# Kernel tuning notes

Measured on AMD Instinct MI355X. Metric: run time of the kernel, lower is better.

Reference implementation:

```python
import jax, jax.numpy as jnp
import numpy as np
from jax import lax

VOCAB, EMB, FILT, ATT, KW = 50000, 300, 400, 200, 3
B, N = 4096, 30

def setup_inputs() -> dict:
    key = jax.random.key(0)
    ks = jax.random.split(key, 7)
    encoded_title = jax.random.randint(ks[0], (B, N), 0, VOCAB)
    emb = jax.random.normal(ks[1], (VOCAB, EMB), dtype=jnp.float32) * 0.1
    conv_w = jax.random.normal(ks[2], (FILT, EMB, KW), dtype=jnp.float32) * (1.0 / np.sqrt(EMB * KW))
    conv_b = jnp.zeros((FILT,), dtype=jnp.float32)
    v = jax.random.normal(ks[3], (FILT, ATT), dtype=jnp.float32) * (1.0 / np.sqrt(FILT))
    vb = jnp.zeros((ATT,), dtype=jnp.float32)
    q = jax.random.normal(ks[4], (ATT, 1), dtype=jnp.float32) * (1.0 / np.sqrt(ATT))
    return {"encoded_title": encoded_title, "emb": emb, "conv_w": conv_w,
            "conv_b": conv_b, "v": v, "vb": vb, "q": q}

def reference(encoded_title, emb, conv_w, conv_b, v, vb, q):
    mask = (encoded_title != 0).astype(jnp.float32)          # [B, N]
    W = emb[encoded_title]                                    # [B, N, E]
    x = jnp.transpose(W, (0, 2, 1))                           # [B, E, N]
    C = lax.conv_general_dilated(x, conv_w, window_strides=(1,),
                                 padding=[(1, 1)],
                                 dimension_numbers=("NCH", "OIH", "NCH"))
    C = jnp.transpose(C, (0, 2, 1)) + conv_b                  # [B, N, F]
    C = jax.nn.relu(C)
    a = jnp.tanh(C @ v + vb)                                  # [B, N, A]
    a = (a @ q)[..., 0]                                       # [B, N]
    alpha = jax.nn.softmax(a, axis=0)                         # softmax over batch dim (faithful to dim=0)
    alpha = alpha * mask
    e = jnp.einsum("bn,bnf->bf", alpha, C)                    # batched weighted-sum pooling
    return e
```

## Files before the change

kernel.cpp:

```cpp
#include <hip/hip_runtime.h>
#include <hip/hip_bf16.h>

#define VOCAB 50000
#define EMB   300
#define FILT  400
#define ATT   200
#define BB    4096
#define NN    30

#define ATTP  208
#define KC    416

typedef short bf16x8 __attribute__((ext_vector_type(8)));
typedef float f32x4  __attribute__((ext_vector_type(4)));
typedef unsigned short u16x4 __attribute__((ext_vector_type(4)));

static __device__ __forceinline__ unsigned short f2bf(float f) {
    __hip_bfloat16 h = __float2bfloat16(f);
    union { __hip_bfloat16 h; unsigned short u; } c; c.h = h; return c.u;
}
static __device__ __forceinline__ float bf2f(unsigned short u) {
    union { unsigned int u; float f; } c; c.u = ((unsigned int)u) << 16; return c.f;
}
static __device__ __forceinline__ float fast_tanh(float x) {
    float e = __expf(2.f * x);
    return 1.f - 2.f * __builtin_amdgcn_rcpf(e + 1.f);
}

static __device__ __forceinline__ void dma16(const unsigned short* g, unsigned short* l) {
    __builtin_amdgcn_global_load_lds(
        (const __attribute__((address_space(1))) unsigned int*)(const void*)g,
        (__attribute__((address_space(3))) unsigned int*)(void*)l,
        16, 0, 0);
}

#define CFENCE() asm volatile("" ::: "memory")
static __device__ __forceinline__ void bar_lgkm0() {
    asm volatile("s_waitcnt lgkmcnt(0)" ::: "memory");
    __builtin_amdgcn_s_barrier();
    CFENCE();
}
static __device__ __forceinline__ void bar_plain() {
    CFENCE();
    __builtin_amdgcn_s_barrier();
    CFENCE();
}

__global__ __launch_bounds__(256) void kP(const float* __restrict__ conv_w,
                                          const float* __restrict__ v,
                                          const float* __restrict__ vb,
                                          const float* __restrict__ q,
                                          unsigned short* __restrict__ Bc2,
                                          unsigned short* __restrict__ Bv2,
                                          float* __restrict__ vbp,
                                          float* __restrict__ qp) {
    int t = blockIdx.x * 256 + threadIdx.x;
    const int NBC = 750 * 512;
    if (t < NBC) {
        int tau = t >> 9, off = t & 511;
        int l = off >> 3, j = off & 7;
        int lm = l & 15, qq = l >> 4;
        int ft = tau % 25, es = (tau / 25) % 10, k = tau / 250;
        int f = ft * 16 + lm;
        int e = es * 32 + qq * 8 + j;
        float val = (e < EMB) ? conv_w[((size_t)f * EMB + e) * 3 + k] : 0.f;
        Bc2[t] = f2bf(val);
    } else {
        int t2 = t - NBC;
        if (t2 < 169 * 512) {
            int tau = t2 >> 9, off = t2 & 511;
            int l = off >> 3, j = off & 7;
            int lm = l & 15, qq = l >> 4;
            int ks = tau / 13, at = tau % 13;
            int att = at * 16 + lm;
            int fcol = ks * 32 + qq * 8 + j;
            float val = (att < ATT && fcol < FILT) ? v[(size_t)fcol * ATT + att] : 0.f;
            Bv2[t2] = f2bf(val);
        }
    }
    if (t < ATTP) {
        vbp[t] = (t < ATT) ? vb[t] : 0.f;
        qp[t]  = (t < ATT) ? q[t] : 0.f;
    }
}

static __device__ __forceinline__ void gather16(const float* __restrict__ emb,
                                                int tok, int e0, float4* aR4) {
#pragma unroll
    for (int c = 0; c < 4; c++) {
        float4 z; z.x = 0.f; z.y = 0.f; z.z = 0.f; z.w = 0.f;
        int ee = e0 + c * 4;
        if (tok >= 0 && ee < EMB)
            z = *(const float4*)(emb + (size_t)tok * EMB + ee);
        aR4[c] = z;
    }
}

__global__ __launch_bounds__(640, 3) void k1_conv(
    const int* __restrict__ idx,
    const float* __restrict__ emb,
    const unsigned short* __restrict__ Bc2,
    const float* __restrict__ conv_b,
    unsigned short* __restrict__ Cws)
{
    __shared__ unsigned short As[131 * 40];
    __shared__ unsigned short Bs[2 * 25 * 512];
    const int bid = blockIdx.x;
    const int t = threadIdx.x;
    const int lane = t & 63, wave = t >> 6;
    const int lm = lane & 15, qq = lane >> 4;
    const int wg = wave / 5, fw = wave % 5;
    const int rbase = wg * 64;
    const bool stager = (wave < 5);

    const int g = t - 320;
    const int uj = g >> 1, uh = g & 1;
    const bool gact = (!stager) && (g < 262);
    int utok = -1;
    if (gact && uj < 128) {
        int ub = uj >> 5, uj2 = uj & 31;
        if (uj2 >= 1 && uj2 <= 30) utok = idx[(bid * 4 + ub) * NN + (uj2 - 1)];
    }

    float4 aR4[4];
    if (stager) {
#pragma unroll
        for (int s = 0; s < 2; s++) {
#pragma unroll
            for (int nt = 0; nt < 5; nt++) {
                int gt = s * 250 + fw * 5 + nt;
                dma16(Bc2 + (size_t)gt * 512 + lane * 8,
                      Bs + s * 12800 + (fw * 5 + nt) * 512);
            }
        }
        asm volatile("s_waitcnt vmcnt(5)" ::: "memory");
    } else if (gact) {
        gather16(emb, utok, uh * 16, aR4);
    }

    f32x4 acc[4][5];
#pragma unroll
    for (int mt = 0; mt < 4; mt++)
#pragma unroll
        for (int nt = 0; nt < 5; nt++)
            acc[mt][nt] = (f32x4){0.f, 0.f, 0.f, 0.f};

    for (int es = 0; es < 10; ++es) {
        if (gact) {
            const float* af = (const float*)aR4;
            union { bf16x8 v; unsigned short u[8]; } cv0, cv1;
#pragma unroll
            for (int jj = 0; jj < 8; jj++) { cv0.u[jj] = f2bf(af[jj]); cv1.u[jj] = f2bf(af[8 + jj]); }
            *(bf16x8*)(As + uj * 40 + uh * 16) = cv0.v;
            *(bf16x8*)(As + uj * 40 + uh * 16 + 8) = cv1.v;
        }
        bar_lgkm0();
        if (gact && es < 9)
            gather16(emb, utok, (es + 1) * 32 + uh * 16, aR4);

#pragma unroll
        for (int k = 0; k < 3; ++k) {
            const int s = es * 3 + k;
            const unsigned short* bb = Bs + (s & 1) * 12800;
            bf16x8 aF[4];
#pragma unroll
            for (int mt = 0; mt < 4; mt++)
                aF[mt] = *(const bf16x8*)(As + (rbase + mt * 16 + lm + k) * 40 + qq * 8);
#pragma unroll
            for (int nt = 0; nt < 5; nt++) {
                bf16x8 bF = *(const bf16x8*)(bb + (fw * 5 + nt) * 512 + lane * 8);
#pragma unroll
                for (int mt = 0; mt < 4; mt++)
                    acc[mt][nt] = __builtin_amdgcn_mfma_f32_16x16x32_bf16(aF[mt], bF, acc[mt][nt], 0, 0, 0);
            }
            bar_lgkm0();
            if (stager) {
                if (k == 0 || es < 9) {
                    const int s2 = s + 2, es2 = s2 / 3, k2 = s2 - es2 * 3;
#pragma unroll
                    for (int nt = 0; nt < 5; nt++) {
                        int gt = (k2 * 10 + es2) * 25 + fw * 5 + nt;
                        dma16(Bc2 + (size_t)gt * 512 + lane * 8,
                              Bs + (s & 1) * 12800 + (fw * 5 + nt) * 512);
                    }
                    asm volatile("s_waitcnt vmcnt(5)" ::: "memory");
                } else {
                    asm volatile("s_waitcnt vmcnt(0)" ::: "memory");
                }
            }
            bar_plain();
        }
    }

    const int f0 = fw * 80;
    float cb[5];
#pragma unroll
    for (int nt = 0; nt < 5; nt++) cb[nt] = conv_b[f0 + nt * 16 + lm];
#pragma unroll
    for (int mt = 0; mt < 4; mt++) {
#pragma unroll
        for (int r = 0; r < 4; r++) {
            int lrow = rbase + mt * 16 + qq * 4 + r;
            int n = lrow & 31;
            int bglob = bid * 4 + (lrow >> 5);
            if (n < NN) {
#pragma unroll
                for (int nt = 0; nt < 5; nt++) {
                    float vv = fmaxf(acc[mt][nt][r] + cb[nt], 0.f);
                    Cws[((size_t)bglob * NN + n) * FILT + f0 + nt * 16 + lm] = f2bf(vv);
                }
            }
        }
    }
}

__global__ __launch_bounds__(256, 3) void k2_att(
    const unsigned short* __restrict__ Cws,
    const unsigned short* __restrict__ Bv2,
    const float* __restrict__ vbp, const float* __restrict__ qp,
    float* __restrict__ a_out)
{
    __shared__ unsigned short Bs[2 * 13 * 512];
    const int lane = threadIdx.x & 63;
    const int wave = threadIdx.x >> 6;
    const int lm = lane & 15, qq = lane >> 4;
    const int r0 = blockIdx.x * 128 + wave * 32;

#pragma unroll
    for (int s = 0; s < 2; s++)
#pragma unroll
        for (int nt = 0; nt < 13; nt++)
            if ((nt & 3) == wave)
                dma16(Bv2 + (size_t)(s * 13 + nt) * 512 + lane * 8,
                      Bs + s * 6656 + nt * 512);

    bf16x8 aFc[2], aFn[2];
#pragma unroll
    for (int mt = 0; mt < 2; mt++)
        aFc[mt] = *(const bf16x8*)(Cws + (size_t)(r0 + mt * 16 + lm) * FILT + 8 * qq);

    f32x4 acc[2][13];
#pragma unroll
    for (int mt = 0; mt < 2; mt++)
#pragma unroll
        for (int nt = 0; nt < 13; nt++) acc[mt][nt] = (f32x4){0.f, 0.f, 0.f, 0.f};

    __syncthreads();

    for (int ks = 0; ks < 13; ++ks) {
        if (ks < 12)
#pragma unroll
            for (int mt = 0; mt < 2; mt++)
                aFn[mt] = *(const bf16x8*)(Cws + (size_t)(r0 + mt * 16 + lm) * FILT + (ks + 1) * 32 + 8 * qq);
        const unsigned short* bb = Bs + (ks & 1) * 6656;
#pragma unroll
        for (int nt = 0; nt < 13; nt++) {
            bf16x8 bF = *(const bf16x8*)(bb + nt * 512 + lane * 8);
#pragma unroll
            for (int mt = 0; mt < 2; mt++)
                acc[mt][nt] = __builtin_amdgcn_mfma_f32_16x16x32_bf16(aFc[mt], bF, acc[mt][nt], 0, 0, 0);
        }
        __syncthreads();
        if (ks + 2 < 13)
#pragma unroll
            for (int nt = 0; nt < 13; nt++)
                if ((nt & 3) == wave)
                    dma16(Bv2 + (size_t)((ks + 2) * 13 + nt) * 512 + lane * 8,
                          Bs + (ks & 1) * 6656 + nt * 512);
#pragma unroll
        for (int mt = 0; mt < 2; mt++) aFc[mt] = aFn[mt];
    }

#pragma unroll
    for (int mt = 0; mt < 2; mt++) {
        float rs[4] = {0.f, 0.f, 0.f, 0.f};
#pragma unroll
        for (int nt = 0; nt < 13; nt++) {
            int att = nt * 16 + lm;
            float vbv = vbp[att], qv = qp[att];
#pragma unroll
            for (int r = 0; r < 4; r++)
                rs[r] += fast_tanh(acc[mt][nt][r] + vbv) * qv;
        }
#pragma unroll
        for (int off = 1; off < 16; off <<= 1)
#pragma unroll
            for (int r = 0; r < 4; r++) rs[r] += __shfl_xor(rs[r], off, 64);
        if (lm == 0) {
#pragma unroll
            for (int r = 0; r < 4; r++) {
                int rg = r0 + mt * 16 + qq * 4 + r;
                a_out[(size_t)(rg % NN) * BB + (rg / NN)] = rs[r];
            }
        }
    }
}

__global__ __launch_bounds__(1024) void k3_softmax(float* __restrict__ a,
                                                   const int* __restrict__ idx) {
    int n = blockIdx.x, tid = threadIdx.x;
    float4 v4 = *(const float4*)(a + (size_t)n * BB + tid * 4);
    float m = fmaxf(fmaxf(v4.x, v4.y), fmaxf(v4.z, v4.w));
    __shared__ float red[32];
#pragma unroll
    for (int off = 32; off >= 1; off >>= 1) m = fmaxf(m, __shfl_xor(m, off, 64));
    int wv = tid >> 6;
    if ((tid & 63) == 0) red[wv] = m;
    __syncthreads();
#pragma unroll
    for (int w = 0; w < 16; w++) m = fmaxf(m, red[w]);
    float e0 = expf(v4.x - m), e1 = expf(v4.y - m);
    float e2 = expf(v4.z - m), e3 = expf(v4.w - m);
    float s = e0 + e1 + e2 + e3;
#pragma unroll
    for (int off = 32; off >= 1; off >>= 1) s += __shfl_xor(s, off, 64);
    if ((tid & 63) == 0) red[16 + wv] = s;
    __syncthreads();
    s = 0.f;
#pragma unroll
    for (int w = 0; w < 16; w++) s += red[16 + w];
    float inv = 1.f / s;
    int b0 = tid * 4;
    float4 o;
    o.x = e0 * inv * ((idx[(size_t)(b0 + 0) * NN + n] != 0) ? 1.f : 0.f);
    o.y = e1 * inv * ((idx[(size_t)(b0 + 1) * NN + n] != 0) ? 1.f : 0.f);
    o.z = e2 * inv * ((idx[(size_t)(b0 + 2) * NN + n] != 0) ? 1.f : 0.f);
    o.w = e3 * inv * ((idx[(size_t)(b0 + 3) * NN + n] != 0) ? 1.f : 0.f);
    *(float4*)(a + (size_t)n * BB + b0) = o;
}

__global__ __launch_bounds__(128) void k4_pool(
    const float* __restrict__ alpha, const unsigned short* __restrict__ C,
    float* __restrict__ out)
{
    int b = blockIdx.x;
    int tid = threadIdx.x;
    __shared__ float al[NN];
    if (tid < NN) al[tid] = alpha[(size_t)tid * BB + b];
    __syncthreads();
    if (tid < 100) {
        int f = tid * 4;
        float s0 = 0.f, s1 = 0.f, s2 = 0.f, s3 = 0.f;
        const unsigned short* Cb = C + (size_t)b * (NN * FILT) + f;
#pragma unroll
        for (int n = 0; n < NN; n++) {
            u16x4 c = *(const u16x4*)(Cb + (size_t)n * FILT);
            float a = al[n];
            s0 = fmaf(a, bf2f(c[0]), s0);
            s1 = fmaf(a, bf2f(c[1]), s1);
            s2 = fmaf(a, bf2f(c[2]), s2);
            s3 = fmaf(a, bf2f(c[3]), s3);
        }
        float4 o; o.x = s0; o.y = s1; o.z = s2; o.w = s3;
        *(float4*)(out + (size_t)b * FILT + f) = o;
    }
}

extern "C" void kernel_launch(void* const* d_in, const int* in_sizes, int n_in,
                              void* d_out, int out_size, void* d_ws, size_t ws_size,
                              hipStream_t stream) {
    const int*   idx    = (const int*)d_in[0];
    const float* emb    = (const float*)d_in[1];
    const float* conv_w = (const float*)d_in[2];
    const float* conv_b = (const float*)d_in[3];
    const float* v      = (const float*)d_in[4];
    const float* vb     = (const float*)d_in[5];
    const float* q      = (const float*)d_in[6];
    float* out = (float*)d_out;

    char* ws = (char*)d_ws;
    size_t o = 0;
    unsigned short* Bv2 = (unsigned short*)(ws + o); o += (size_t)169 * 512 * 2;
    float* vbp = (float*)(ws + o);                   o += 1024;
    float* qp  = (float*)(ws + o);                   o += 1024;
    unsigned short* Bc2 = (unsigned short*)(ws + o);
    float* a_buf = (float*)(ws + o);
    o += (size_t)750 * 512 * 2;
    unsigned short* Cws = (unsigned short*)(ws + o);

    const int NP = 750 * 512 + 169 * 512;
    kP<<<(NP + 255) / 256, 256, 0, stream>>>(conv_w, v, vb, q, Bc2, Bv2, vbp, qp);
    k1_conv<<<BB / 4, 640, 0, stream>>>(idx, emb, Bc2, conv_b, Cws);
    k2_att<<<(BB * NN) / 128, 256, 0, stream>>>(Cws, Bv2, vbp, qp, a_buf);
    k3_softmax<<<NN, 1024, 0, stream>>>(a_buf, idx);
    k4_pool<<<BB, 128, 0, stream>>>(a_buf, Cws, out);
}
```

Baseline: 269.4 us.

## Triple-buffer conv weights, double-buffer A tile, fold softmax normalize into pooling

The conv kernel now keeps three B-weight stage buffers and two A-embedding buffers in dynamic shared memory. Each k-step needs one barrier instead of two, and the gathers are issued further ahead of their use. The softmax kernel now only writes the per-position max and sum, and the pooling kernel computes the masked exp weights itself, so one write-and-reread pass over the alpha buffer is gone. The cost is about 96KB of LDS per block, which may lower occupancy below the 3 blocks per CU the launch bounds target.

```diff
diff --git a/kernel.cpp b/kernel.cpp
--- a/kernel.cpp
+++ b/kernel.cpp
@@ -37,11 +37,6 @@
 #define CFENCE() asm volatile("" ::: "memory")
 static __device__ __forceinline__ void bar_lgkm0() {
     asm volatile("s_waitcnt lgkmcnt(0)" ::: "memory");
-    __builtin_amdgcn_s_barrier();
-    CFENCE();
-}
-static __device__ __forceinline__ void bar_plain() {
-    CFENCE();
     __builtin_amdgcn_s_barrier();
     CFENCE();
 }
@@ -96,6 +91,16 @@
     }
 }
 
+static __device__ __forceinline__ void publishA(unsigned short* Ab, int uj, int uh,
+                                                const float4* aR4) {
+    const float* af = (const float*)aR4;
+    union { bf16x8 v; unsigned short u[8]; } cv0, cv1;
+#pragma unroll
+    for (int jj = 0; jj < 8; jj++) { cv0.u[jj] = f2bf(af[jj]); cv1.u[jj] = f2bf(af[8 + jj]); }
+    *(bf16x8*)(Ab + uj * 40 + uh * 16) = cv0.v;
+    *(bf16x8*)(Ab + uj * 40 + uh * 16 + 8) = cv1.v;
+}
+
 __global__ __launch_bounds__(640, 3) void k1_conv(
     const int* __restrict__ idx,
     const float* __restrict__ emb,
@@ -103,8 +108,10 @@
     const float* __restrict__ conv_b,
     unsigned short* __restrict__ Cws)
 {
-    __shared__ unsigned short As[131 * 40];
-    __shared__ unsigned short Bs[2 * 25 * 512];
+    extern __shared__ unsigned short sh[];
+    unsigned short* const Bs = sh;
+    unsigned short* const As = sh + 38400;
+
     const int bid = blockIdx.x;
     const int t = threadIdx.x;
     const int lane = t & 63, wave = t >> 6;
@@ -125,17 +132,21 @@
     float4 aR4[4];
     if (stager) {
 #pragma unroll
-        for (int s = 0; s < 2; s++) {
+        for (int s = 0; s < 3; s++) {
 #pragma unroll
             for (int nt = 0; nt < 5; nt++) {
-                int gt = s * 250 + fw * 5 + nt;
+                int gt = (s * 10) * 25 + fw * 5 + nt;
                 dma16(Bc2 + (size_t)gt * 512 + lane * 8,
                       Bs + s * 12800 + (fw * 5 + nt) * 512);
             }
         }
-        asm volatile("s_waitcnt vmcnt(5)" ::: "memory");
+        asm volatile("s_waitcnt vmcnt(10)" ::: "memory");
     } else if (gact) {
-        gather16(emb, utok, uh * 16, aR4);
+        gather16(emb, utok, 0 + uh * 16, aR4);
+        publishA(As, uj, uh, aR4);
+        gather16(emb, utok, 32 + uh * 16, aR4);
+        publishA(As + 5240, uj, uh, aR4);
+        gather16(emb, utok, 64 + uh * 16, aR4);
     }
 
     f32x4 acc[4][5];
@@ -145,27 +156,17 @@
         for (int nt = 0; nt < 5; nt++)
             acc[mt][nt] = (f32x4){0.f, 0.f, 0.f, 0.f};
 
+    bar_lgkm0();
+
     for (int es = 0; es < 10; ++es) {
-        if (gact) {
-            const float* af = (const float*)aR4;
-            union { bf16x8 v; unsigned short u[8]; } cv0, cv1;
-#pragma unroll
-            for (int jj = 0; jj < 8; jj++) { cv0.u[jj] = f2bf(af[jj]); cv1.u[jj] = f2bf(af[8 + jj]); }
-            *(bf16x8*)(As + uj * 40 + uh * 16) = cv0.v;
-            *(bf16x8*)(As + uj * 40 + uh * 16 + 8) = cv1.v;
-        }
-        bar_lgkm0();
-        if (gact && es < 9)
-            gather16(emb, utok, (es + 1) * 32 + uh * 16, aR4);
-
+        const unsigned short* Ab = As + (es & 1) * 5240;
 #pragma unroll
         for (int k = 0; k < 3; ++k) {
-            const int s = es * 3 + k;
-            const unsigned short* bb = Bs + (s & 1) * 12800;
+            const unsigned short* bb = Bs + k * 12800;
             bf16x8 aF[4];
 #pragma unroll
             for (int mt = 0; mt < 4; mt++)
-                aF[mt] = *(const bf16x8*)(As + (rbase + mt * 16 + lm + k) * 40 + qq * 8);
+                aF[mt] = *(const bf16x8*)(Ab + (rbase + mt * 16 + lm + k) * 40 + qq * 8);
 #pragma unroll
             for (int nt = 0; nt < 5; nt++) {
                 bf16x8 bF = *(const bf16x8*)(bb + (fw * 5 + nt) * 512 + lane * 8);
@@ -173,22 +174,25 @@
                 for (int mt = 0; mt < 4; mt++)
                     acc[mt][nt] = __builtin_amdgcn_mfma_f32_16x16x32_bf16(aF[mt], bF, acc[mt][nt], 0, 0, 0);
             }
-            bar_lgkm0();
+            if (k == 0 && gact && es >= 1 && es <= 8) {
+                publishA(As + ((es + 1) & 1) * 5240, uj, uh, aR4);
+                if (es <= 7) gather16(emb, utok, (es + 2) * 32 + uh * 16, aR4);
+            }
             if (stager) {
-                if (k == 0 || es < 9) {
-                    const int s2 = s + 2, es2 = s2 / 3, k2 = s2 - es2 * 3;
-#pragma unroll
-                    for (int nt = 0; nt < 5; nt++) {
-                        int gt = (k2 * 10 + es2) * 25 + fw * 5 + nt;
-                        dma16(Bc2 + (size_t)gt * 512 + lane * 8,
-                              Bs + (s & 1) * 12800 + (fw * 5 + nt) * 512);
-                    }
+                if (es < 9 || k == 0)
                     asm volatile("s_waitcnt vmcnt(5)" ::: "memory");
-                } else {
+                else if (k == 1)
                     asm volatile("s_waitcnt vmcnt(0)" ::: "memory");
+            }
+            if (es < 9 || k < 2) bar_lgkm0();
+            if (stager && es < 9) {
+#pragma unroll
+                for (int nt = 0; nt < 5; nt++) {
+                    int gt = (k * 10 + es + 1) * 25 + fw * 5 + nt;
+                    dma16(Bc2 + (size_t)gt * 512 + lane * 8,
+                          Bs + k * 12800 + (fw * 5 + nt) * 512);
                 }
             }
-            bar_plain();
         }
     }
 
@@ -296,8 +300,8 @@
     }
 }
 
-__global__ __launch_bounds__(1024) void k3_softmax(float* __restrict__ a,
-                                                   const int* __restrict__ idx) {
+__global__ __launch_bounds__(1024) void k3_stats(const float* __restrict__ a,
+                                                 float* __restrict__ mS) {
     int n = blockIdx.x, tid = threadIdx.x;
     float4 v4 = *(const float4*)(a + (size_t)n * BB + tid * 4);
     float m = fmaxf(fmaxf(v4.x, v4.y), fmaxf(v4.z, v4.w));
@@ -319,24 +323,22 @@
     s = 0.f;
 #pragma unroll
     for (int w = 0; w < 16; w++) s += red[16 + w];
-    float inv = 1.f / s;
-    int b0 = tid * 4;
-    float4 o;
-    o.x = e0 * inv * ((idx[(size_t)(b0 + 0) * NN + n] != 0) ? 1.f : 0.f);
-    o.y = e1 * inv * ((idx[(size_t)(b0 + 1) * NN + n] != 0) ? 1.f : 0.f);
-    o.z = e2 * inv * ((idx[(size_t)(b0 + 2) * NN + n] != 0) ? 1.f : 0.f);
-    o.w = e3 * inv * ((idx[(size_t)(b0 + 3) * NN + n] != 0) ? 1.f : 0.f);
-    *(float4*)(a + (size_t)n * BB + b0) = o;
+    if (tid == 0) { mS[n] = m; mS[NN + n] = s; }
 }
 
 __global__ __launch_bounds__(128) void k4_pool(
-    const float* __restrict__ alpha, const unsigned short* __restrict__ C,
+    const float* __restrict__ a, const float* __restrict__ mS,
+    const int* __restrict__ idx, const unsigned short* __restrict__ C,
     float* __restrict__ out)
 {
     int b = blockIdx.x;
     int tid = threadIdx.x;
     __shared__ float al[NN];
-    if (tid < NN) al[tid] = alpha[(size_t)tid * BB + b];
+    if (tid < NN) {
+        float av = a[(size_t)tid * BB + b];
+        float msk = (idx[(size_t)b * NN + tid] != 0) ? 1.f : 0.f;
+        al[tid] = expf(av - mS[tid]) * (1.f / mS[NN + tid]) * msk;
+    }
     __syncthreads();
     if (tid < 100) {
         int f = tid * 4;
@@ -345,11 +347,11 @@
 #pragma unroll
         for (int n = 0; n < NN; n++) {
             u16x4 c = *(const u16x4*)(Cb + (size_t)n * FILT);
-            float a = al[n];
-            s0 = fmaf(a, bf2f(c[0]), s0);
-            s1 = fmaf(a, bf2f(c[1]), s1);
-            s2 = fmaf(a, bf2f(c[2]), s2);
-            s3 = fmaf(a, bf2f(c[3]), s3);
+            float aa = al[n];
+            s0 = fmaf(aa, bf2f(c[0]), s0);
+            s1 = fmaf(aa, bf2f(c[1]), s1);
+            s2 = fmaf(aa, bf2f(c[2]), s2);
+            s3 = fmaf(aa, bf2f(c[3]), s3);
         }
         float4 o; o.x = s0; o.y = s1; o.z = s2; o.w = s3;
         *(float4*)(out + (size_t)b * FILT + f) = o;
@@ -373,15 +375,23 @@
     unsigned short* Bv2 = (unsigned short*)(ws + o); o += (size_t)169 * 512 * 2;
     float* vbp = (float*)(ws + o);                   o += 1024;
     float* qp  = (float*)(ws + o);                   o += 1024;
+    float* mS  = (float*)(ws + o);                   o += 1024;
     unsigned short* Bc2 = (unsigned short*)(ws + o);
     float* a_buf = (float*)(ws + o);
     o += (size_t)750 * 512 * 2;
     unsigned short* Cws = (unsigned short*)(ws + o);
 
+    static bool s_attr_set = false;
+    if (!s_attr_set) {
+        hipFuncSetAttribute(reinterpret_cast<const void*>(k1_conv),
+                            hipFuncAttributeMaxDynamicSharedMemorySize, 98304);
+        s_attr_set = true;
+    }
+
     const int NP = 750 * 512 + 169 * 512;
     kP<<<(NP + 255) / 256, 256, 0, stream>>>(conv_w, v, vb, q, Bc2, Bv2, vbp, qp);
-    k1_conv<<<BB / 4, 640, 0, stream>>>(idx, emb, Bc2, conv_b, Cws);
+    k1_conv<<<BB / 4, 640, 97760, stream>>>(idx, emb, Bc2, conv_b, Cws);
     k2_att<<<(BB * NN) / 128, 256, 0, stream>>>(Cws, Bv2, vbp, qp, a_buf);
-    k3_softmax<<<NN, 1024, 0, stream>>>(a_buf, idx);
-    k4_pool<<<BB, 128, 0, stream>>>(a_buf, Cws, out);
-}
+    k3_stats<<<NN, 1024, 0, stream>>>(a_buf, mS);
+    k4_pool<<<BB, 128, 0, stream>>>(a_buf, mS, idx, Cws, out);
+}
```

New measurement: 269.9 us. No clear change (+0.2%).
